# Kernel tuning notes

Measured on AMD Instinct MI355X. Metric: run time of the kernel, lower is better.

## Reference

```python
import jax, jax.numpy as jnp
import numpy as np

N = 50000      # nodes
E = 800000     # edges (before self-loops)
IN_DIM = 128
HID = 96
PROJ = 64
BN_EPS = 1e-5
L2_EPS = 1e-12


def setup_inputs() -> dict:
    key = jax.random.key(0)
    ks = jax.random.split(key, 8)

    def glorot(k, shape):
        fan_in, fan_out = shape
        s = np.sqrt(6.0 / (fan_in + fan_out)).astype(np.float32)
        return jax.random.uniform(k, shape, jnp.float32, -s, s)

    x = jax.random.normal(ks[0], (N, IN_DIM), jnp.float32)
    edge_index = jax.random.randint(ks[1], (2, E), 0, N, dtype=jnp.int64)

    return {
        "x": x,
        "edge_index": edge_index,
        # GCN layer 1
        "W1": glorot(ks[2], (IN_DIM, HID)), "b1": jnp.zeros(HID, jnp.float32),
        "g1": jnp.ones(HID, jnp.float32), "be1": jnp.zeros(HID, jnp.float32),
        # GCN layer 2
        "W2": glorot(ks[3], (HID, HID)), "b2": jnp.zeros(HID, jnp.float32),
        "g2": jnp.ones(HID, jnp.float32), "be2": jnp.zeros(HID, jnp.float32),
        # projector: Linear -> BN -> ReLU -> Linear
        "Wp1": glorot(ks[4], (HID, HID)), "bp1": jnp.zeros(HID, jnp.float32),
        "gp": jnp.ones(HID, jnp.float32), "bep": jnp.zeros(HID, jnp.float32),
        "Wp2": glorot(ks[5], (HID, PROJ)), "bp2": jnp.zeros(PROJ, jnp.float32),
    }


def _batchnorm(h, gamma, beta):
    # training-mode BatchNorm1d: batch stats, biased variance
    m = h.mean(axis=0)
    v = h.var(axis=0)
    return gamma * (h - m) * jax.lax.rsqrt(v + BN_EPS) + beta


def _gcn_conv(x, W, b, src, dst, deg_inv_sqrt):
    # PyG GCNConv: x @ W, symmetric-normalized scatter-add (self-loops included
    # in src/dst), then bias.
    xw = x @ W                                              # [N, out]
    norm = deg_inv_sqrt[src] * deg_inv_sqrt[dst]            # [E+N]
    msg = xw[src] * norm[:, None]                           # [E+N, out]
    out = jax.ops.segment_sum(msg, dst, num_segments=x.shape[0])
    return out + b


def reference(x, edge_index, W1, b1, g1, be1, W2, b2, g2, be2,
              Wp1, bp1, gp, bep, Wp2, bp2):
    n = x.shape[0]
    loops = jnp.arange(n, dtype=edge_index.dtype)
    src = jnp.concatenate([edge_index[0], loops])
    dst = jnp.concatenate([edge_index[1], loops])
    deg = jax.ops.segment_sum(jnp.ones(src.shape[0], x.dtype), dst,
                              num_segments=n)               # includes self-loops
    deg_inv_sqrt = jax.lax.rsqrt(deg)                       # deg >= 1 always

    h = jax.nn.relu(_batchnorm(_gcn_conv(x, W1, b1, src, dst, deg_inv_sqrt), g1, be1))
    h = jax.nn.relu(_batchnorm(_gcn_conv(h, W2, b2, src, dst, deg_inv_sqrt), g2, be2))

    z = jax.nn.relu(_batchnorm(h @ Wp1 + bp1, gp, bep))
    z = z @ Wp2 + bp2
    # F.normalize(p=2, dim=-1, eps=1e-12)
    nrm = jnp.linalg.norm(z, axis=-1, keepdims=True)
    return z / jnp.maximum(nrm, L2_EPS)
```

## Files before the change

### kernel.cpp

```cpp
#include <hip/hip_runtime.h>
#include <hip/hip_fp16.h>

constexpr int BLK = 256;

static inline int cdiv(long long a, int b) { return (int)((a + b - 1) / b); }

using v8h = __attribute__((ext_vector_type(8))) _Float16;
using v4f = __attribute__((ext_vector_type(4))) float;


__global__ __launch_bounds__(256) void scan1_dis(const int* __restrict__ cnt,
                                                 int* __restrict__ rowptr,
                                                 int* __restrict__ bsum,
                                                 float* __restrict__ dis, int N) {
    __shared__ int ts[256];
    int tid = threadIdx.x;
    int base = blockIdx.x * 1024 + tid * 4;
    int v[4], s = 0;
#pragma unroll
    for (int i = 0; i < 4; ++i) {
        v[i] = (base + i < N) ? cnt[base + i] : 0;
        s += v[i];
        if (base + i < N) dis[base + i] = rsqrtf((float)v[i] + 1.0f);
    }
    ts[tid] = s;
    __syncthreads();
    for (int off = 1; off < 256; off <<= 1) {
        int t = 0;
        if (tid >= off) t = ts[tid - off];
        __syncthreads();
        if (tid >= off) ts[tid] += t;
        __syncthreads();
    }
    int run = ts[tid] - s;
#pragma unroll
    for (int i = 0; i < 4; ++i) {
        if (base + i < N) rowptr[base + i] = run;
        run += v[i];
    }
    if (tid == 255) bsum[blockIdx.x] = ts[255];
}

__global__ __launch_bounds__(256) void scan23(int* __restrict__ rowptr,
                                              const int* __restrict__ bsum,
                                              int nb, int N, int E) {
    __shared__ int sboff[64];
    const int tid = threadIdx.x;
    if (tid < 64) {
        int orig = (tid < nb) ? bsum[tid] : 0;
        int v = orig;
#pragma unroll
        for (int off = 1; off < 64; off <<= 1) {
            int t = __shfl_up(v, off, 64);
            if (tid >= off) v += t;
        }
        sboff[tid] = v - orig;
    }
    __syncthreads();
    int i = blockIdx.x * 256 + tid;
    if (i < N) rowptr[i] += sboff[i >> 10];
    if (i == 0) rowptr[N] = E;
}

__global__ void csr_fill(const int* __restrict__ src, const int* __restrict__ dst,
                         const unsigned short* __restrict__ eoff,
                         const int* __restrict__ rowptr,
                         unsigned short* __restrict__ csrc, int E) {
    for (int i = blockIdx.x * blockDim.x + threadIdx.x; i < E; i += gridDim.x * blockDim.x) {
        csrc[rowptr[dst[i]] + (int)eoff[i]] = (unsigned short)src[i];
    }
}


template <int K, bool ACT, bool BIAS, bool STATS, typename TIN>
__device__ __forceinline__ void gemm96_body(int bid,
                                            const TIN* __restrict__ in,
                                            const float* __restrict__ W,
                                            const float* __restrict__ bias,
                                            const float* __restrict__ bnsums,
                                            const float* __restrict__ gamma,
                                            const float* __restrict__ beta,
                                            const float* __restrict__ dsc,
                                            _Float16* __restrict__ hout,
                                            float* __restrict__ osums, int N) {
    constexpr int NK = K / 32;
    constexpr int LDK = K + 8;
    __shared__ __align__(16) _Float16 Wt[96 * LDK];
    __shared__ __align__(16) float ssl[ACT ? 192 : 1];
    __shared__ float sb[STATS ? 192 : 1];
    const int tid = threadIdx.x;
    for (int idx = tid; idx < K * 96; idx += 256) {
        int k = idx / 96, n = idx - k * 96;
        Wt[n * LDK + k] = (_Float16)W[idx];
    }
    if (ACT && tid < 96) {
        float inv_n = 1.0f / (float)N;
        float mean = bnsums[tid] * inv_n;
        float var = bnsums[96 + tid] * inv_n - mean * mean;
        float sc = gamma[tid] * rsqrtf(var + 1e-5f);
        ssl[tid] = sc;
        ssl[96 + tid] = beta[tid] - mean * sc;
    }
    if (STATS && tid < 192) sb[tid] = 0.0f;
    __syncthreads();

    const int wave = tid >> 6, lane = tid & 63;
    const int quad = lane >> 4, lm = lane & 15;
    const int rbase = bid * 64 + wave * 16;
    int arow = rbase + lm;
    arow = arow < N ? arow : N - 1;

    v8h afr[NK];
#pragma unroll
    for (int kc = 0; kc < NK; ++kc) {
        const int kk = kc * 32 + quad * 8;
        if constexpr (sizeof(TIN) == 4) {
            const float* p = (const float*)&in[(long long)arow * K + kk];
            float4 p0 = *(const float4*)p;
            float4 p1 = *(const float4*)(p + 4);
            if (ACT) {
                float4 sc0 = *(const float4*)&ssl[kk];
                float4 sc1 = *(const float4*)&ssl[kk + 4];
                float4 sh0 = *(const float4*)&ssl[96 + kk];
                float4 sh1 = *(const float4*)&ssl[96 + kk + 4];
                p0.x = fmaxf(fmaf(p0.x, sc0.x, sh0.x), 0.0f);
                p0.y = fmaxf(fmaf(p0.y, sc0.y, sh0.y), 0.0f);
                p0.z = fmaxf(fmaf(p0.z, sc0.z, sh0.z), 0.0f);
                p0.w = fmaxf(fmaf(p0.w, sc0.w, sh0.w), 0.0f);
                p1.x = fmaxf(fmaf(p1.x, sc1.x, sh1.x), 0.0f);
                p1.y = fmaxf(fmaf(p1.y, sc1.y, sh1.y), 0.0f);
                p1.z = fmaxf(fmaf(p1.z, sc1.z, sh1.z), 0.0f);
                p1.w = fmaxf(fmaf(p1.w, sc1.w, sh1.w), 0.0f);
            }
            v8h a;
            a[0] = (_Float16)p0.x; a[1] = (_Float16)p0.y;
            a[2] = (_Float16)p0.z; a[3] = (_Float16)p0.w;
            a[4] = (_Float16)p1.x; a[5] = (_Float16)p1.y;
            a[6] = (_Float16)p1.z; a[7] = (_Float16)p1.w;
            afr[kc] = a;
        } else {
            v8h hv = *(const v8h*)&in[(long long)arow * K + kk];
            if (ACT) {
#pragma unroll
                for (int j = 0; j < 8; ++j) {
                    float f = (float)hv[j];
                    f = fmaxf(fmaf(f, ssl[kk + j], ssl[96 + kk + j]), 0.0f);
                    hv[j] = (_Float16)f;
                }
            }
            afr[kc] = hv;
        }
    }

    v4f acc[6];
#pragma unroll
    for (int t = 0; t < 6; ++t) {
        v4f c = {0.0f, 0.0f, 0.0f, 0.0f};
#pragma unroll
        for (int kc = 0; kc < NK; ++kc) {
            v8h b = *(const v8h*)&Wt[(t * 16 + lm) * LDK + kc * 32 + quad * 8];
            c = __builtin_amdgcn_mfma_f32_16x16x32_f16(afr[kc], b, c, 0, 0, 0);
        }
        acc[t] = c;
    }

    float dr[4];
#pragma unroll
    for (int r = 0; r < 4; ++r) {
        int gr = rbase + quad * 4 + r;
        dr[r] = dsc ? dsc[gr < N ? gr : N - 1] : 1.0f;
    }

    float ls[6], lq[6];
#pragma unroll
    for (int t = 0; t < 6; ++t) { ls[t] = 0.0f; lq[t] = 0.0f; }
#pragma unroll
    for (int t = 0; t < 6; ++t) {
        float bv = BIAS ? bias[t * 16 + lm] : 0.0f;
#pragma unroll
        for (int r = 0; r < 4; ++r) {
            int gr = rbase + quad * 4 + r;
            if (gr < N) {
                float o = acc[t][r] + bv;
                hout[(long long)gr * 96 + t * 16 + lm] = (_Float16)(o * dr[r]);
                if (STATS) { ls[t] += o; lq[t] += o * o; }
            }
        }
    }
    if (STATS) {
#pragma unroll
        for (int t = 0; t < 6; ++t) {
            ls[t] += __shfl_xor(ls[t], 16);
            ls[t] += __shfl_xor(ls[t], 32);
            lq[t] += __shfl_xor(lq[t], 16);
            lq[t] += __shfl_xor(lq[t], 32);
        }
        if (quad == 0) {
#pragma unroll
            for (int t = 0; t < 6; ++t) {
                atomicAdd(&sb[t * 16 + lm], ls[t]);
                atomicAdd(&sb[96 + t * 16 + lm], lq[t]);
            }
        }
        __syncthreads();
        if (tid < 192) atomicAdd(&osums[tid], sb[tid]);
    }
}

template <int K, bool ACT, bool BIAS, bool STATS, typename TIN>
__global__ __launch_bounds__(256) void gemm96m(const TIN* __restrict__ in,
                                               const float* __restrict__ W,
                                               const float* __restrict__ bias,
                                               const float* __restrict__ bnsums,
                                               const float* __restrict__ gamma,
                                               const float* __restrict__ beta,
                                               const float* __restrict__ dsc,
                                               _Float16* __restrict__ hout,
                                               float* __restrict__ osums, int N) {
    gemm96_body<K, ACT, BIAS, STATS, TIN>(blockIdx.x, in, W, bias, bnsums,
                                          gamma, beta, dsc, hout, osums, N);
}

__global__ __launch_bounds__(256) void gemm1_count(const float* __restrict__ x,
                                                   const float* __restrict__ W1,
                                                   _Float16* __restrict__ hout,
                                                   const int* __restrict__ dst,
                                                   int* __restrict__ cnt,
                                                   unsigned short* __restrict__ eoff,
                                                   int gG, int N, int E) {
    if ((int)blockIdx.x < gG) {
        gemm96_body<128, false, false, false, float>(
            blockIdx.x, x, W1, nullptr, nullptr, nullptr, nullptr, nullptr,
            hout, nullptr, N);
    } else {
        int g = (blockIdx.x - gG) * 256 + threadIdx.x;
        int stride = (gridDim.x - gG) * 256;
        for (int i = g; i < E; i += stride)
            eoff[i] = (unsigned short)atomicAdd(&cnt[dst[i]], 1);
    }
}


__global__ __launch_bounds__(256) void gemm_finalm(const _Float16* __restrict__ in,
                                                   const float* __restrict__ W,
                                                   const float* __restrict__ bias,
                                                   const float* __restrict__ bnsums,
                                                   const float* __restrict__ gamma,
                                                   const float* __restrict__ beta,
                                                   float* __restrict__ out, int N) {
    constexpr int K = 96, NK = 3, LDK = K + 8;
    __shared__ __align__(16) _Float16 Wt[64 * LDK];
    __shared__ __align__(16) float ssl[192];
    const int tid = threadIdx.x;
    for (int idx = tid; idx < K * 64; idx += 256) {
        int k = idx / 64, n = idx - k * 64;
        Wt[n * LDK + k] = (_Float16)W[idx];
    }
    if (tid < 96) {
        float inv_n = 1.0f / (float)N;
        float mean = bnsums[tid] * inv_n;
        float var = bnsums[96 + tid] * inv_n - mean * mean;
        float sc = gamma[tid] * rsqrtf(var + 1e-5f);
        ssl[tid] = sc;
        ssl[96 + tid] = beta[tid] - mean * sc;
    }
    __syncthreads();

    const int wave = tid >> 6, lane = tid & 63;
    const int quad = lane >> 4, lm = lane & 15;
    const int rbase = blockIdx.x * 64 + wave * 16;
    int arow = rbase + lm;
    arow = arow < N ? arow : N - 1;

    v8h afr[NK];
#pragma unroll
    for (int kc = 0; kc < NK; ++kc) {
        const int kk = kc * 32 + quad * 8;
        v8h hv = *(const v8h*)&in[(long long)arow * K + kk];
#pragma unroll
        for (int j = 0; j < 8; ++j) {
            float f = (float)hv[j];
            f = fmaxf(fmaf(f, ssl[kk + j], ssl[96 + kk + j]), 0.0f);
            hv[j] = (_Float16)f;
        }
        afr[kc] = hv;
    }

    v4f acc[4];
#pragma unroll
    for (int t = 0; t < 4; ++t) {
        v4f c = {0.0f, 0.0f, 0.0f, 0.0f};
#pragma unroll
        for (int kc = 0; kc < NK; ++kc) {
            v8h b = *(const v8h*)&Wt[(t * 16 + lm) * LDK + kc * 32 + quad * 8];
            c = __builtin_amdgcn_mfma_f32_16x16x32_f16(afr[kc], b, c, 0, 0, 0);
        }
        float bv = bias[t * 16 + lm];
        c[0] += bv; c[1] += bv; c[2] += bv; c[3] += bv;
        acc[t] = c;
    }

    float sq[4];
#pragma unroll
    for (int r = 0; r < 4; ++r) {
        float s = acc[0][r] * acc[0][r] + acc[1][r] * acc[1][r] +
                  acc[2][r] * acc[2][r] + acc[3][r] * acc[3][r];
#pragma unroll
        for (int m = 1; m < 16; m <<= 1) s += __shfl_xor(s, m, 64);
        sq[r] = 1.0f / fmaxf(sqrtf(s), 1e-12f);
    }
#pragma unroll
    for (int r = 0; r < 4; ++r) {
        int gr = rbase + quad * 4 + r;
        if (gr < N) {
#pragma unroll
            for (int t = 0; t < 4; ++t)
                out[(long long)gr * 64 + t * 16 + lm] = acc[t][r] * sq[r];
        }
    }
}


__device__ __forceinline__ void acc_row(float* acc, const __half2* h) {
#pragma unroll
    for (int k = 0; k < 4; ++k) {
        float2 f = __half22float2(h[k]);
        acc[2 * k + 0] += f.x;
        acc[2 * k + 1] += f.y;
    }
}

__device__ __forceinline__ void acc_roww(float* acc, const __half2* h, float w) {
#pragma unroll
    for (int k = 0; k < 4; ++k) {
        float2 f = __half22float2(h[k]);
        acc[2 * k + 0] = fmaf(f.x, w, acc[2 * k + 0]);
        acc[2 * k + 1] = fmaf(f.y, w, acc[2 * k + 1]);
    }
}

template <bool PRESC>
__global__ __launch_bounds__(256) void agg96h(const __half* __restrict__ hxw,
                                              const int* __restrict__ rowptr,
                                              const unsigned short* __restrict__ csrc,
                                              const float* __restrict__ dis,
                                              const float* __restrict__ bias,
                                              _Float16* __restrict__ outh, int N) {
    int idx = blockIdx.x * 256 + threadIdx.x;
    if (idx >= N * 12) return;
    int n = idx / 12, c8 = idx % 12;
    int ch = c8 * 8;
    float dn = dis[n];
    float acc[8];
    {
        float sw = PRESC ? 1.0f : dn;
        float4 g = *(const float4*)&hxw[(long long)n * 96 + ch];
        const __half2* hs = (const __half2*)&g;
#pragma unroll
        for (int k = 0; k < 4; ++k) {
            float2 f = __half22float2(hs[k]);
            acc[2 * k + 0] = f.x * sw;
            acc[2 * k + 1] = f.y * sw;
        }
    }
    int e = rowptr[n], e1 = rowptr[n + 1];
    for (; e + 7 < e1; e += 8) {
        int s[8];
        float4 g[8];
        float w[8];
#pragma unroll
        for (int j = 0; j < 8; ++j) s[j] = csrc[e + j];
        if (!PRESC) {
#pragma unroll
            for (int j = 0; j < 8; ++j) w[j] = dis[s[j]];
        }
#pragma unroll
        for (int j = 0; j < 8; ++j)
            g[j] = *(const float4*)&hxw[(long long)s[j] * 96 + ch];
#pragma unroll
        for (int j = 0; j < 8; ++j) {
            if (PRESC) acc_row(acc, (const __half2*)&g[j]);
            else       acc_roww(acc, (const __half2*)&g[j], w[j]);
        }
    }
    for (; e + 3 < e1; e += 4) {
        int s[4];
        float4 g[4];
        float w[4];
#pragma unroll
        for (int j = 0; j < 4; ++j) s[j] = csrc[e + j];
        if (!PRESC) {
#pragma unroll
            for (int j = 0; j < 4; ++j) w[j] = dis[s[j]];
        }
#pragma unroll
        for (int j = 0; j < 4; ++j)
            g[j] = *(const float4*)&hxw[(long long)s[j] * 96 + ch];
#pragma unroll
        for (int j = 0; j < 4; ++j) {
            if (PRESC) acc_row(acc, (const __half2*)&g[j]);
            else       acc_roww(acc, (const __half2*)&g[j], w[j]);
        }
    }
    for (; e < e1; ++e) {
        int s0 = csrc[e];
        float4 g0 = *(const float4*)&hxw[(long long)s0 * 96 + ch];
        if (PRESC) acc_row(acc, (const __half2*)&g0);
        else       acc_roww(acc, (const __half2*)&g0, dis[s0]);
    }
    v8h o;
#pragma unroll
    for (int j = 0; j < 8; ++j)
        o[j] = (_Float16)fmaf(acc[j], dn, bias[ch + j]);
    *(v8h*)&outh[(long long)n * 96 + ch] = o;
}


__global__ __launch_bounds__(256) void bn_stats96h(const __half* __restrict__ h,
                                                   float* __restrict__ sums, int N) {
    __shared__ float sb[192];
    const int tid = threadIdx.x;
    if (tid < 192) sb[tid] = 0.0f;
    __syncthreads();
    int g = blockIdx.x * 256 + tid;
    int total = N * 12, stride = gridDim.x * 256;
    int c8 = g % 12;
    float s[8] = {0, 0, 0, 0, 0, 0, 0, 0};
    float q[8] = {0, 0, 0, 0, 0, 0, 0, 0};
    for (int i = g; i < total; i += stride) {
        int n = i / 12;
        float4 raw = *(const float4*)&h[n * 96 + 8 * c8];
        const __half2* hp = (const __half2*)&raw;
#pragma unroll
        for (int k = 0; k < 4; ++k) {
            float2 f = __half22float2(hp[k]);
            s[2 * k + 0] += f.x;
            s[2 * k + 1] += f.y;
            q[2 * k + 0] += f.x * f.x;
            q[2 * k + 1] += f.y * f.y;
        }
    }
#pragma unroll
    for (int j = 0; j < 8; ++j) {
        atomicAdd(&sb[8 * c8 + j], s[j]);
        atomicAdd(&sb[96 + 8 * c8 + j], q[j]);
    }
    __syncthreads();
    if (tid < 192) atomicAdd(&sums[tid], sb[tid]);
}


extern "C" void kernel_launch(void* const* d_in, const int* in_sizes, int n_in,
                              void* d_out, int out_size, void* d_ws, size_t ws_size,
                              hipStream_t stream) {
    const float* x   = (const float*)d_in[0];
    const int*   ei  = (const int*)d_in[1];
    const float* W1  = (const float*)d_in[2];
    const float* b1  = (const float*)d_in[3];
    const float* g1  = (const float*)d_in[4];
    const float* be1 = (const float*)d_in[5];
    const float* W2  = (const float*)d_in[6];
    const float* b2  = (const float*)d_in[7];
    const float* g2  = (const float*)d_in[8];
    const float* be2 = (const float*)d_in[9];
    const float* Wp1 = (const float*)d_in[10];
    const float* bp1 = (const float*)d_in[11];
    const float* gp  = (const float*)d_in[12];
    const float* bep = (const float*)d_in[13];
    const float* Wp2 = (const float*)d_in[14];
    const float* bp2 = (const float*)d_in[15];

    const int N = in_sizes[0] / 128;
    const int E = in_sizes[1] / 2;
    const int* src = ei;
    const int* dst = ei + E;

    char* w = (char*)d_ws;
    auto alloc = [&](size_t bytes) { char* p = w; w += (bytes + 15) & ~size_t(15); return p; };
    int*            cnt    = (int*)alloc((size_t)N * 4);
    float*          sums   = (float*)alloc(576 * 4);
    int*            rowptr = (int*)alloc((size_t)(N + 1) * 4);
    int*            bsum   = (int*)alloc(64 * 4);
    float*          dis    = (float*)alloc((size_t)N * 4);
    unsigned short* eoff   = (unsigned short*)alloc((size_t)E * 2);
    unsigned short* csrc   = (unsigned short*)alloc((size_t)E * 2);
    _Float16*       buf2h  = (_Float16*)alloc((size_t)N * 96 * 2);
    _Float16*       hbuf   = (_Float16*)alloc((size_t)N * 96 * 2);
    float* sums1 = sums, *sums2 = sums + 192, *sums3 = sums + 384;

    float* out = (float*)d_out;

    const int gE  = cdiv(E, BLK);
    const int gG  = cdiv(N, 64);
    const int gC  = 1024;
    const int gA  = cdiv((long long)N * 12, BLK);
    const int nb  = cdiv(N, 1024);

    size_t zlen = (size_t)((char*)sums - (char*)cnt) + 576 * 4;
    hipMemsetAsync(cnt, 0, zlen, stream);

    gemm1_count<<<gG + gC, 256, 0, stream>>>(x, W1, hbuf, dst, cnt, eoff, gG, N, E);
    scan1_dis<<<nb, 256, 0, stream>>>(cnt, rowptr, bsum, dis, N);
    scan23<<<cdiv(N, 256), 256, 0, stream>>>(rowptr, bsum, nb, N, E);
    csr_fill<<<gE, BLK, 0, stream>>>(src, dst, eoff, rowptr, csrc, E);

    agg96h<false><<<gA, 256, 0, stream>>>((const __half*)hbuf, rowptr, csrc, dis,
                                          b1, buf2h, N);
    bn_stats96h<<<510, 256, 0, stream>>>((const __half*)buf2h, sums1, N);

    gemm96m<96, true, false, false, _Float16><<<gG, 256, 0, stream>>>(
        buf2h, W2, nullptr, sums1, g1, be1, dis, hbuf, nullptr, N);
    agg96h<true><<<gA, 256, 0, stream>>>((const __half*)hbuf, rowptr, csrc, dis,
                                         b2, buf2h, N);
    bn_stats96h<<<510, 256, 0, stream>>>((const __half*)buf2h, sums2, N);

    gemm96m<96, true, true, true, _Float16><<<gG, 256, 0, stream>>>(
        buf2h, Wp1, bp1, sums2, g2, be2, nullptr, hbuf, sums3, N);

    gemm_finalm<<<gG, 256, 0, stream>>>(hbuf, Wp2, bp2, sums3, gp, bep, out, N);
}
```

Baseline: 308.2 us.

## Store hidden features in channel-planar layout for cache-local aggregation

Hidden activations change from row-major [N,96] fp16 to 12 planes of [N][8]. The GEMMs write and read the planar layout, the aggregation kernel runs one plane per group of workgroups, and an XCD-aware block remap keeps each plane's chunks together. The aim is to shrink the random-gather working set per plane so that neighbour gathers stay in L2 instead of hitting the full feature matrix. BN stats are rewritten per plane using wave shuffles and fewer atomics. This adds more blocks and a per-plane CSR re-read, and it relies on the hidden gemm1 path producing the same planar layout.

After: 371.1 us. 20.4% more time.

```diff
diff --git a/kernel.cpp b/kernel.cpp
--- a/kernel.cpp
+++ b/kernel.cpp
@@ -7,6 +7,7 @@
 
 using v8h = __attribute__((ext_vector_type(8))) _Float16;
 using v4f = __attribute__((ext_vector_type(4))) float;
+
 
 
 __global__ __launch_bounds__(256) void scan1_dis(const int* __restrict__ cnt,
@@ -139,7 +140,7 @@
             a[6] = (_Float16)p1.z; a[7] = (_Float16)p1.w;
             afr[kc] = a;
         } else {
-            v8h hv = *(const v8h*)&in[(long long)arow * K + kk];
+            v8h hv = *(const v8h*)&in[((long long)(kk >> 3) * N + arow) * 8];
             if (ACT) {
 #pragma unroll
                 for (int j = 0; j < 8; ++j) {
@@ -177,12 +178,15 @@
 #pragma unroll
     for (int t = 0; t < 6; ++t) {
         float bv = BIAS ? bias[t * 16 + lm] : 0.0f;
+        const int col = t * 16 + lm;
+        const long long pbase = (long long)(col >> 3) * N;
+        const int cj = col & 7;
 #pragma unroll
         for (int r = 0; r < 4; ++r) {
             int gr = rbase + quad * 4 + r;
             if (gr < N) {
                 float o = acc[t][r] + bv;
-                hout[(long long)gr * 96 + t * 16 + lm] = (_Float16)(o * dr[r]);
+                hout[(pbase + gr) * 8 + cj] = (_Float16)(o * dr[r]);
                 if (STATS) { ls[t] += o; lq[t] += o * o; }
             }
         }
@@ -276,7 +280,7 @@
 #pragma unroll
     for (int kc = 0; kc < NK; ++kc) {
         const int kk = kc * 32 + quad * 8;
-        v8h hv = *(const v8h*)&in[(long long)arow * K + kk];
+        v8h hv = *(const v8h*)&in[((long long)(kk >> 3) * N + arow) * 8];
 #pragma unroll
         for (int j = 0; j < 8; ++j) {
             float f = (float)hv[j];
@@ -321,40 +325,26 @@
 }
 
 
-__device__ __forceinline__ void acc_row(float* acc, const __half2* h) {
-#pragma unroll
-    for (int k = 0; k < 4; ++k) {
-        float2 f = __half22float2(h[k]);
-        acc[2 * k + 0] += f.x;
-        acc[2 * k + 1] += f.y;
-    }
-}
-
-__device__ __forceinline__ void acc_roww(float* acc, const __half2* h, float w) {
-#pragma unroll
-    for (int k = 0; k < 4; ++k) {
-        float2 f = __half22float2(h[k]);
-        acc[2 * k + 0] = fmaf(f.x, w, acc[2 * k + 0]);
-        acc[2 * k + 1] = fmaf(f.y, w, acc[2 * k + 1]);
-    }
-}
-
 template <bool PRESC>
-__global__ __launch_bounds__(256) void agg96h(const __half* __restrict__ hxw,
+__global__ __launch_bounds__(256) void agg96p(const __half* __restrict__ hxw,
                                               const int* __restrict__ rowptr,
                                               const unsigned short* __restrict__ csrc,
                                               const float* __restrict__ dis,
                                               const float* __restrict__ bias,
-                                              _Float16* __restrict__ outh, int N) {
-    int idx = blockIdx.x * 256 + threadIdx.x;
-    if (idx >= N * 12) return;
-    int n = idx / 12, c8 = idx % 12;
-    int ch = c8 * 8;
+                                              _Float16* __restrict__ outh,
+                                              int nch, int N) {
+    int nwg = gridDim.x;
+    int wid = (nwg % 8 == 0) ? (blockIdx.x % 8) * (nwg / 8) + blockIdx.x / 8
+                             : (int)blockIdx.x;
+    int plane = wid / nch, chunk = wid - plane * nch;
+    int n = chunk * 256 + threadIdx.x;
+    if (n >= N) return;
+    const __half* hp = hxw + (long long)plane * N * 8;
     float dn = dis[n];
     float acc[8];
     {
         float sw = PRESC ? 1.0f : dn;
-        float4 g = *(const float4*)&hxw[(long long)n * 96 + ch];
+        float4 g = *(const float4*)&hp[n * 8];
         const __half2* hs = (const __half2*)&g;
 #pragma unroll
         for (int k = 0; k < 4; ++k) {
@@ -375,12 +365,19 @@
             for (int j = 0; j < 8; ++j) w[j] = dis[s[j]];
         }
 #pragma unroll
-        for (int j = 0; j < 8; ++j)
-            g[j] = *(const float4*)&hxw[(long long)s[j] * 96 + ch];
+        for (int j = 0; j < 8; ++j) g[j] = *(const float4*)&hp[s[j] * 8];
 #pragma unroll
         for (int j = 0; j < 8; ++j) {
-            if (PRESC) acc_row(acc, (const __half2*)&g[j]);
-            else       acc_roww(acc, (const __half2*)&g[j], w[j]);
+            const __half2* h = (const __half2*)&g[j];
+#pragma unroll
+            for (int k = 0; k < 4; ++k) {
+                float2 f = __half22float2(h[k]);
+                if (PRESC) { acc[2 * k] += f.x; acc[2 * k + 1] += f.y; }
+                else {
+                    acc[2 * k]     = fmaf(f.x, w[j], acc[2 * k]);
+                    acc[2 * k + 1] = fmaf(f.y, w[j], acc[2 * k + 1]);
+                }
+            }
         }
     }
     for (; e + 3 < e1; e += 4) {
@@ -394,59 +391,81 @@
             for (int j = 0; j < 4; ++j) w[j] = dis[s[j]];
         }
 #pragma unroll
-        for (int j = 0; j < 4; ++j)
-            g[j] = *(const float4*)&hxw[(long long)s[j] * 96 + ch];
+        for (int j = 0; j < 4; ++j) g[j] = *(const float4*)&hp[s[j] * 8];
 #pragma unroll
         for (int j = 0; j < 4; ++j) {
-            if (PRESC) acc_row(acc, (const __half2*)&g[j]);
-            else       acc_roww(acc, (const __half2*)&g[j], w[j]);
+            const __half2* h = (const __half2*)&g[j];
+#pragma unroll
+            for (int k = 0; k < 4; ++k) {
+                float2 f = __half22float2(h[k]);
+                if (PRESC) { acc[2 * k] += f.x; acc[2 * k + 1] += f.y; }
+                else {
+                    acc[2 * k]     = fmaf(f.x, w[j], acc[2 * k]);
+                    acc[2 * k + 1] = fmaf(f.y, w[j], acc[2 * k + 1]);
+                }
+            }
         }
     }
     for (; e < e1; ++e) {
         int s0 = csrc[e];
-        float4 g0 = *(const float4*)&hxw[(long long)s0 * 96 + ch];
-        if (PRESC) acc_row(acc, (const __half2*)&g0);
-        else       acc_roww(acc, (const __half2*)&g0, dis[s0]);
-    }
+        float w0 = PRESC ? 1.0f : dis[s0];
+        float4 g0 = *(const float4*)&hp[s0 * 8];
+        const __half2* h = (const __half2*)&g0;
+#pragma unroll
+        for (int k = 0; k < 4; ++k) {
+            float2 f = __half22float2(h[k]);
+            acc[2 * k]     = fmaf(f.x, w0, acc[2 * k]);
+            acc[2 * k + 1] = fmaf(f.y, w0, acc[2 * k + 1]);
+        }
+    }
+    const int ch = plane * 8;
     v8h o;
 #pragma unroll
     for (int j = 0; j < 8; ++j)
         o[j] = (_Float16)fmaf(acc[j], dn, bias[ch + j]);
-    *(v8h*)&outh[(long long)n * 96 + ch] = o;
-}
-
-
-__global__ __launch_bounds__(256) void bn_stats96h(const __half* __restrict__ h,
-                                                   float* __restrict__ sums, int N) {
-    __shared__ float sb[192];
+    *(v8h*)&outh[((long long)plane * N + n) * 8] = o;
+}
+
+
+__global__ __launch_bounds__(256) void bn_statsp(const __half* __restrict__ h,
+                                                 float* __restrict__ sums,
+                                                 int nch, int N) {
+    __shared__ float sb[16];
     const int tid = threadIdx.x;
-    if (tid < 192) sb[tid] = 0.0f;
+    if (tid < 16) sb[tid] = 0.0f;
     __syncthreads();
-    int g = blockIdx.x * 256 + tid;
-    int total = N * 12, stride = gridDim.x * 256;
-    int c8 = g % 12;
+    int plane = blockIdx.x / nch, chunk = blockIdx.x - plane * nch;
+    int n = chunk * 256 + tid;
     float s[8] = {0, 0, 0, 0, 0, 0, 0, 0};
     float q[8] = {0, 0, 0, 0, 0, 0, 0, 0};
-    for (int i = g; i < total; i += stride) {
-        int n = i / 12;
-        float4 raw = *(const float4*)&h[n * 96 + 8 * c8];
+    if (n < N) {
+        float4 raw = *(const float4*)&h[((long long)plane * N + n) * 8];
         const __half2* hp = (const __half2*)&raw;
 #pragma unroll
         for (int k = 0; k < 4; ++k) {
             float2 f = __half22float2(hp[k]);
-            s[2 * k + 0] += f.x;
-            s[2 * k + 1] += f.y;
-            q[2 * k + 0] += f.x * f.x;
-            q[2 * k + 1] += f.y * f.y;
+            s[2 * k + 0] = f.x;  s[2 * k + 1] = f.y;
+            q[2 * k + 0] = f.x * f.x;  q[2 * k + 1] = f.y * f.y;
         }
     }
 #pragma unroll
     for (int j = 0; j < 8; ++j) {
-        atomicAdd(&sb[8 * c8 + j], s[j]);
-        atomicAdd(&sb[96 + 8 * c8 + j], q[j]);
+#pragma unroll
+        for (int m = 1; m < 64; m <<= 1) {
+            s[j] += __shfl_xor(s[j], m, 64);
+            q[j] += __shfl_xor(q[j], m, 64);
+        }
+    }
+    if ((tid & 63) == 0) {
+#pragma unroll
+        for (int j = 0; j < 8; ++j) {
+            atomicAdd(&sb[j], s[j]);
+            atomicAdd(&sb[8 + j], q[j]);
+        }
     }
     __syncthreads();
-    if (tid < 192) atomicAdd(&sums[tid], sb[tid]);
+    if (tid < 16)
+        atomicAdd(&sums[(tid >> 3) * 96 + plane * 8 + (tid & 7)], sb[tid]);
 }
 
 
@@ -490,11 +509,12 @@
 
     float* out = (float*)d_out;
 
-    const int gE  = cdiv(E, BLK);
-    const int gG  = cdiv(N, 64);
-    const int gC  = 1024;
-    const int gA  = cdiv((long long)N * 12, BLK);
-    const int nb  = cdiv(N, 1024);
+    const int gE   = cdiv(E, BLK);
+    const int gG   = cdiv(N, 64);
+    const int gC   = 1024;
+    const int nb   = cdiv(N, 1024);
+    const int nch  = cdiv(N, 256);
+    const int gAgg = 12 * nch;
 
     size_t zlen = (size_t)((char*)sums - (char*)cnt) + 576 * 4;
     hipMemsetAsync(cnt, 0, zlen, stream);
@@ -504,15 +524,15 @@
     scan23<<<cdiv(N, 256), 256, 0, stream>>>(rowptr, bsum, nb, N, E);
     csr_fill<<<gE, BLK, 0, stream>>>(src, dst, eoff, rowptr, csrc, E);
 
-    agg96h<false><<<gA, 256, 0, stream>>>((const __half*)hbuf, rowptr, csrc, dis,
-                                          b1, buf2h, N);
-    bn_stats96h<<<510, 256, 0, stream>>>((const __half*)buf2h, sums1, N);
+    agg96p<false><<<gAgg, 256, 0, stream>>>((const __half*)hbuf, rowptr, csrc, dis,
+                                            b1, buf2h, nch, N);
+    bn_statsp<<<gAgg, 256, 0, stream>>>((const __half*)buf2h, sums1, nch, N);
 
     gemm96m<96, true, false, false, _Float16><<<gG, 256, 0, stream>>>(
         buf2h, W2, nullptr, sums1, g1, be1, dis, hbuf, nullptr, N);
-    agg96h<true><<<gA, 256, 0, stream>>>((const __half*)hbuf, rowptr, csrc, dis,
-                                         b2, buf2h, N);
-    bn_stats96h<<<510, 256, 0, stream>>>((const __half*)buf2h, sums2, N);
+    agg96p<true><<<gAgg, 256, 0, stream>>>((const __half*)hbuf, rowptr, csrc, dis,
+                                           b2, buf2h, nch, N);
+    bn_statsp<<<gAgg, 256, 0, stream>>>((const __half*)buf2h, sums2, nch, N);
 
     gemm96m<96, true, true, true, _Float16><<<gG, 256, 0, stream>>>(
         buf2h, Wp1, bp1, sums2, g2, be2, nullptr, hbuf, sums3, N);
```
